# Kernel optimization log

Hardware: AMD Instinct MI355X
Metric: run time of the kernel (lower is better)

Reference implementation:

```python
import jax, jax.numpy as jnp
import numpy as np


def setup_inputs() -> dict:
    key = jax.random.key(0)
    k = jax.random.split(key, 6)
    B, S, L, V = 512, 256, 128, 32000
    words = jax.random.randint(k[0], (B, S), 0, V)
    encoder_emits = jax.random.normal(k[1], (B, S, L), dtype=jnp.float32)
    mask = jnp.ones((B, S), dtype=bool)  # token 0 always valid; all-valid lengths here
    feature_table = jax.random.normal(k[2], (V, L), dtype=jnp.float32)
    start = jax.random.normal(k[3], (L,), dtype=jnp.float32)
    transitions = jax.random.normal(k[4], (L, L), dtype=jnp.float32)
    end = jax.random.normal(k[5], (L,), dtype=jnp.float32)
    return {"words": words, "encoder_emits": encoder_emits, "mask": mask,
            "feature_table": feature_table, "start": start,
            "transitions": transitions, "end": end}


def reference(words, encoder_emits, mask, feature_table, start, transitions, end):
    # decoder emits: feature_scorer(words) modeled as per-word label-score lookup
    dec = feature_table[words]                       # [B, S, L]
    # init at t = 0
    log_alpha = start[None, :] + encoder_emits[:, 0]  # [B, L]
    log_beta = log_alpha + dec[:, 0]                  # [B, L]

    def step(carry, xs):
        la, lb = carry
        e_i, d_i, m_i = xs                            # [B,L], [B,L], [B]
        crf = e_i[:, None, :] + transitions[None]     # [B, L, L] (prev, cur)
        a_new = jax.nn.logsumexp(la[:, :, None] + crf, axis=1)
        b_new = jax.nn.logsumexp(lb[:, :, None] + crf + d_i[:, None, :], axis=1)
        m = m_i[:, None]
        return (jnp.where(m, a_new, la), jnp.where(m, b_new, lb)), None

    xs = (jnp.swapaxes(encoder_emits[:, 1:], 0, 1),   # [S-1, B, L]
          jnp.swapaxes(dec[:, 1:], 0, 1),
          mask[:, 1:].T)                              # [S-1, B]
    (log_alpha, log_beta), _ = jax.lax.scan(step, (log_alpha, log_beta), xs)

    la = jax.nn.logsumexp(log_alpha + end[None, :], axis=-1)  # [B]
    lb = jax.nn.logsumexp(log_beta + end[None, :], axis=-1)   # [B]
    return (la - lb).sum()
```

## Files before the change

kernel.cpp:

```cpp
#include <hip/hip_runtime.h>


constexpr int SS  = 256;
constexpr int LL  = 128;
constexpr int BST = 136;

typedef _Float16 half2_t __attribute__((ext_vector_type(2)));
typedef _Float16 half4_t __attribute__((ext_vector_type(4)));
typedef _Float16 half8_t __attribute__((ext_vector_type(8)));
typedef float    f32x4   __attribute__((ext_vector_type(4)));
typedef unsigned uint2_t __attribute__((ext_vector_type(2)));

#define MFMA16(a, b, c) __builtin_amdgcn_mfma_f32_16x16x32_f16((a), (b), (c), 0, 0, 0)
#define PKRTZ(a, b) __builtin_bit_cast(half2_t, __builtin_amdgcn_cvt_pkrtz((a), (b)))

#define BAR() do {                                                \
    asm volatile("s_waitcnt lgkmcnt(0)" ::: "memory");            \
    __builtin_amdgcn_s_barrier();                                 \
    asm volatile("" ::: "memory");                                \
} while (0)

__device__ __forceinline__ float quad_allmax(float x) {
#if __has_builtin(__builtin_amdgcn_permlane16_swap) && __has_builtin(__builtin_amdgcn_permlane32_swap)
    unsigned u = __builtin_bit_cast(unsigned, x);
    uint2_t a = __builtin_amdgcn_permlane16_swap(u, u, false, false);
    float m = fmaxf(__builtin_bit_cast(float, a.x), __builtin_bit_cast(float, a.y));
    unsigned v = __builtin_bit_cast(unsigned, m);
    uint2_t b = __builtin_amdgcn_permlane32_swap(v, v, false, false);
    return fmaxf(__builtin_bit_cast(float, b.x), __builtin_bit_cast(float, b.y));
#else
    x = fmaxf(x, __shfl_xor(x, 16, 64));
    return fmaxf(x, __shfl_xor(x, 32, 64));
#endif
}

__global__ __launch_bounds__(256) void prepass(
    const int* __restrict__ words, const float* __restrict__ emits,
    const float* __restrict__ ftab,
    half4_t* __restrict__ xe, half4_t* __restrict__ xb,
    float* __restrict__ out)
{
    if (blockIdx.x == 0 && threadIdx.x == 0) *out = 0.f;
    const int t = threadIdx.x;
    const int R = blockIdx.x * 8 + (t >> 5);
    const int c = t & 31;
    const int w = words[R];
    const f32x4 e = *(const f32x4*)&emits[(size_t)R * LL + 4 * c];
    const f32x4 d = *(const f32x4*)&ftab[(size_t)w * LL + 4 * c];
    half4_t a, bb;
    #pragma unroll
    for (int r = 0; r < 4; ++r) {
        a[r]  = (_Float16)__expf(e[r]);
        bb[r] = (_Float16)__expf(e[r] + d[r]);
    }
    xe[(size_t)R * 32 + c] = a;
    xb[(size_t)R * 32 + c] = bb;
}

#define STEP(i, XS) do {                                                      \
    const int rp_ = ((i) + 1) & 1, wp_ = (i) & 1;                             \
    O2 -= __log2f(invp);             \
    half8_t bf_[4];                                                           \
    _Pragma("unroll")                                                         \
    for (int c = 0; c < 4; ++c)                                               \
        bf_[c] = *(const half8_t*)&P[rp_][m15 * BST + c * 32 + quad * 8];     \
    f32x4 a_ = MFMA16(areg[0], bf_[0], zero4);                                \
    f32x4 b_ = MFMA16(areg[2], bf_[2], zero4);                                \
    a_ = MFMA16(areg[1], bf_[1], a_);                                         \
    b_ = MFMA16(areg[3], bf_[3], b_);                                         \
    const f32x4 y_ = a_ + b_;                                                 \
    const float p0_ = y_[0] * (float)XS[0] * invp;                            \
    const float p1_ = y_[1] * (float)XS[1] * invp;                            \
    const float p2_ = y_[2] * (float)XS[2] * invp;                            \
    const float p3_ = y_[3] * (float)XS[3] * invp;                            \
    {                                                                         \
        half2_t h0_ = PKRTZ(p0_, p1_), h1_ = PKRTZ(p2_, p3_);                 \
        half4_t pa_; pa_[0]=h0_[0]; pa_[1]=h0_[1]; pa_[2]=h1_[0]; pa_[3]=h1_[1];\
        *(half4_t*)&P[wp_][m15 * BST + wave * 16 + col0] = pa_;               \
    }                                                                         \
    const int ipf_ = ((i) + 3 < SS) ? (i) + 3 : SS - 1;                       \
    XS = *(const half4_t*)&X[xrow + (size_t)ipf_ * LL + wave * 16 + col0];    \
    float mm_ = fmaxf(fmaxf(p0_, p1_), fmaxf(p2_, p3_));                      \
    mm_ = quad_allmax(mm_);                                                   \
    if (quad == 0) PM[wp_][m15][wave] = mm_;                                  \
    BAR();                                                                    \
    const f32x4 pmA_ = *(const f32x4*)&PM[wp_][m15][0];                       \
    const f32x4 pmB_ = *(const f32x4*)&PM[wp_][m15][4];                       \
    invp = __builtin_amdgcn_rcpf(                                             \
        fmaxf(fmaxf(fmaxf(pmA_[0], pmA_[1]), fmaxf(pmA_[2], pmA_[3])),        \
              fmaxf(fmaxf(pmB_[0], pmB_[1]), fmaxf(pmB_[2], pmB_[3]))));      \
} while (0)

__global__ __launch_bounds__(512, 1) void crf_scan(
    const float* __restrict__ start,
    const float* __restrict__ trans,
    const float* __restrict__ endv,
    const _Float16* __restrict__ xe,
    const _Float16* __restrict__ xb,
    float* __restrict__ out)
{
    const int blk   = blockIdx.x;
    const int chain = blk & 1;
    const int grp   = blk >> 1;
    const int tid   = threadIdx.x;
    const int wave  = tid >> 6;
    const int lane  = tid & 63;
    const int m15   = lane & 15;
    const int quad  = lane >> 4;
    const int col0  = quad * 4;
    const int batch = grp * 16 + m15;
    const _Float16* __restrict__ X = chain ? xb : xe;

    __shared__ __align__(16) _Float16 P[2][16 * BST];
    __shared__ __align__(16) float    PM[2][16][8];

    half8_t areg[4];
    #pragma unroll
    for (int c = 0; c < 4; ++c)
        #pragma unroll
        for (int jj = 0; jj < 8; ++jj)
            areg[c][jj] = (_Float16)__expf(
                trans[(c * 32 + quad * 8 + jj) * LL + wave * 16 + m15]);

    const size_t xrow = (size_t)batch * SS * LL;
    const f32x4 zero4 = (f32x4){0.f, 0.f, 0.f, 0.f};

    float invp, O2 = 0.f;

    {
        const int s0 = wave * 16 + col0;
        const f32x4  sv = *(const f32x4*)&start[s0];
        const half4_t x0 = *(const half4_t*)&X[xrow + s0];
        float y0 = __expf(sv[0]) * (float)x0[0];
        float y1 = __expf(sv[1]) * (float)x0[1];
        float y2 = __expf(sv[2]) * (float)x0[2];
        float y3 = __expf(sv[3]) * (float)x0[3];
        half2_t h0 = PKRTZ(y0, y1), h1 = PKRTZ(y2, y3);
        half4_t pa; pa[0]=h0[0]; pa[1]=h0[1]; pa[2]=h1[0]; pa[3]=h1[1];
        *(half4_t*)&P[0][m15 * BST + s0] = pa;
        float mm = fmaxf(fmaxf(y0, y1), fmaxf(y2, y3));
        mm = quad_allmax(mm);
        if (quad == 0) PM[0][m15][wave] = mm;
    }
    BAR();
    {
        const f32x4 pmA = *(const f32x4*)&PM[0][m15][0];
        const f32x4 pmB = *(const f32x4*)&PM[0][m15][4];
        invp = __builtin_amdgcn_rcpf(
            fmaxf(fmaxf(fmaxf(pmA[0], pmA[1]), fmaxf(pmA[2], pmA[3])),
                  fmaxf(fmaxf(pmB[0], pmB[1]), fmaxf(pmB[2], pmB[3]))));
    }

    half4_t xA, xB, xC;
    xA = *(const half4_t*)&X[xrow + (size_t)1 * LL + wave * 16 + col0];
    xB = *(const half4_t*)&X[xrow + (size_t)2 * LL + wave * 16 + col0];
    xC = *(const half4_t*)&X[xrow + (size_t)3 * LL + wave * 16 + col0];

    for (int i = 1; i + 2 < SS; i += 3) {
        STEP(i,     xA);
        STEP(i + 1, xB);
        STEP(i + 2, xC);
    }

    if (wave == 0) {
        float s = 0.f;
        #pragma unroll
        for (int t = 0; t < 8; ++t) {
            const half4_t p  = *(const half4_t*)&P[1][m15 * BST + t * 16 + col0];
            const f32x4   ev = *(const f32x4*)&endv[t * 16 + col0];
            #pragma unroll
            for (int r = 0; r < 4; ++r)
                s += (float)p[r] * __expf(ev[r]);
        }
        s += __shfl_xor(s, 16, 64);
        s += __shfl_xor(s, 32, 64);
        float lf = O2 * 0.6931471805599453f + __logf(s);
        if (chain) lf = -lf;
        if (quad == 0) {
            lf += __shfl_xor(lf, 1, 64);
            lf += __shfl_xor(lf, 2, 64);
            lf += __shfl_xor(lf, 4, 64);
            lf += __shfl_xor(lf, 8, 64);
            if (m15 == 0) atomicAdd(out, lf);
        }
    }
}

extern "C" void kernel_launch(void* const* d_in, const int* in_sizes, int n_in,
                              void* d_out, int out_size, void* d_ws, size_t ws_size,
                              hipStream_t stream) {
    const int*   words = (const int*)d_in[0];
    const float* emits = (const float*)d_in[1];
    const float* ftab  = (const float*)d_in[3];
    const float* start = (const float*)d_in[4];
    const float* trans = (const float*)d_in[5];
    const float* endv  = (const float*)d_in[6];
    float* out = (float*)d_out;

    half4_t* xe = (half4_t*)d_ws;
    half4_t* xb = xe + (size_t)512 * SS * 32;

    prepass<<<512 * SS / 8, 256, 0, stream>>>(words, emits, ftab, xe, xb, out);
    crf_scan<<<64, 512, 0, stream>>>(start, trans, endv,
                                     (const _Float16*)xe, (const _Float16*)xb, out);
}
```

Baseline: 222.1 us.

## Split batch across more blocks with four sequences per MFMA tile

Each scan block now handles 4 batch rows instead of 16, and the launch grows from 64 to 256 blocks so more compute units work on the sequential CRF recurrence. The MFMA still runs on 16 rows, with rows replicated modulo 4, so three quarters of the matrix work is redundant but the per-step latency stays about the same. The aim is to use more CUs at once; in exchange the per-batch transition matrix loads and the redundant MFMA work add overhead, and the LDS row stride changes to 144.

```diff
diff --git a/kernel.cpp b/kernel.cpp
--- a/kernel.cpp
+++ b/kernel.cpp
@@ -3,7 +3,8 @@
 
 constexpr int SS  = 256;
 constexpr int LL  = 128;
-constexpr int BST = 136;
+constexpr int BB  = 4;
+constexpr int BST = 144;
 
 typedef _Float16 half2_t __attribute__((ext_vector_type(2)));
 typedef _Float16 half4_t __attribute__((ext_vector_type(4)));
@@ -63,7 +64,7 @@
     half8_t bf_[4];                                                           \
     _Pragma("unroll")                                                         \
     for (int c = 0; c < 4; ++c)                                               \
-        bf_[c] = *(const half8_t*)&P[rp_][m15 * BST + c * 32 + quad * 8];     \
+        bf_[c] = *(const half8_t*)&P[rp_][bsl * BST + c * 32 + quad * 8];     \
     f32x4 a_ = MFMA16(areg[0], bf_[0], zero4);                                \
     f32x4 b_ = MFMA16(areg[2], bf_[2], zero4);                                \
     a_ = MFMA16(areg[1], bf_[1], a_);                                         \
@@ -73,7 +74,7 @@
     const float p1_ = y_[1] * (float)XS[1] * invp;                            \
     const float p2_ = y_[2] * (float)XS[2] * invp;                            \
     const float p3_ = y_[3] * (float)XS[3] * invp;                            \
-    {                                                                         \
+    if (m15 < BB) {                                                           \
         half2_t h0_ = PKRTZ(p0_, p1_), h1_ = PKRTZ(p2_, p3_);                 \
         half4_t pa_; pa_[0]=h0_[0]; pa_[1]=h0_[1]; pa_[2]=h1_[0]; pa_[3]=h1_[1];\
         *(half4_t*)&P[wp_][m15 * BST + wave * 16 + col0] = pa_;               \
@@ -82,10 +83,10 @@
     XS = *(const half4_t*)&X[xrow + (size_t)ipf_ * LL + wave * 16 + col0];    \
     float mm_ = fmaxf(fmaxf(p0_, p1_), fmaxf(p2_, p3_));                      \
     mm_ = quad_allmax(mm_);                                                   \
-    if (quad == 0) PM[wp_][m15][wave] = mm_;                                  \
+    if (quad == 0 && m15 < BB) PM[wp_][m15][wave] = mm_;                      \
     BAR();                                                                    \
-    const f32x4 pmA_ = *(const f32x4*)&PM[wp_][m15][0];                       \
-    const f32x4 pmB_ = *(const f32x4*)&PM[wp_][m15][4];                       \
+    const f32x4 pmA_ = *(const f32x4*)&PM[wp_][bsl][0];                       \
+    const f32x4 pmB_ = *(const f32x4*)&PM[wp_][bsl][4];                       \
     invp = __builtin_amdgcn_rcpf(                                             \
         fmaxf(fmaxf(fmaxf(pmA_[0], pmA_[1]), fmaxf(pmA_[2], pmA_[3])),        \
               fmaxf(fmaxf(pmB_[0], pmB_[1]), fmaxf(pmB_[2], pmB_[3]))));      \
@@ -106,13 +107,14 @@
     const int wave  = tid >> 6;
     const int lane  = tid & 63;
     const int m15   = lane & 15;
+    const int bsl   = m15 & (BB - 1);
     const int quad  = lane >> 4;
     const int col0  = quad * 4;
-    const int batch = grp * 16 + m15;
+    const int batch = grp * BB + bsl;
     const _Float16* __restrict__ X = chain ? xb : xe;
 
-    __shared__ __align__(16) _Float16 P[2][16 * BST];
-    __shared__ __align__(16) float    PM[2][16][8];
+    __shared__ __align__(16) _Float16 P[2][BB * BST];
+    __shared__ __align__(16) float    PM[2][BB][8];
 
     half8_t areg[4];
     #pragma unroll
@@ -135,17 +137,19 @@
         float y1 = __expf(sv[1]) * (float)x0[1];
         float y2 = __expf(sv[2]) * (float)x0[2];
         float y3 = __expf(sv[3]) * (float)x0[3];
-        half2_t h0 = PKRTZ(y0, y1), h1 = PKRTZ(y2, y3);
-        half4_t pa; pa[0]=h0[0]; pa[1]=h0[1]; pa[2]=h1[0]; pa[3]=h1[1];
-        *(half4_t*)&P[0][m15 * BST + s0] = pa;
+        if (m15 < BB) {
+            half2_t h0 = PKRTZ(y0, y1), h1 = PKRTZ(y2, y3);
+            half4_t pa; pa[0]=h0[0]; pa[1]=h0[1]; pa[2]=h1[0]; pa[3]=h1[1];
+            *(half4_t*)&P[0][m15 * BST + s0] = pa;
+        }
         float mm = fmaxf(fmaxf(y0, y1), fmaxf(y2, y3));
         mm = quad_allmax(mm);
-        if (quad == 0) PM[0][m15][wave] = mm;
+        if (quad == 0 && m15 < BB) PM[0][m15][wave] = mm;
     }
     BAR();
     {
-        const f32x4 pmA = *(const f32x4*)&PM[0][m15][0];
-        const f32x4 pmB = *(const f32x4*)&PM[0][m15][4];
+        const f32x4 pmA = *(const f32x4*)&PM[0][bsl][0];
+        const f32x4 pmB = *(const f32x4*)&PM[0][bsl][4];
         invp = __builtin_amdgcn_rcpf(
             fmaxf(fmaxf(fmaxf(pmA[0], pmA[1]), fmaxf(pmA[2], pmA[3])),
                   fmaxf(fmaxf(pmB[0], pmB[1]), fmaxf(pmB[2], pmB[3]))));
@@ -166,7 +170,7 @@
         float s = 0.f;
         #pragma unroll
         for (int t = 0; t < 8; ++t) {
-            const half4_t p  = *(const half4_t*)&P[1][m15 * BST + t * 16 + col0];
+            const half4_t p  = *(const half4_t*)&P[1][bsl * BST + t * 16 + col0];
             const f32x4   ev = *(const f32x4*)&endv[t * 16 + col0];
             #pragma unroll
             for (int r = 0; r < 4; ++r)
@@ -179,8 +183,6 @@
         if (quad == 0) {
             lf += __shfl_xor(lf, 1, 64);
             lf += __shfl_xor(lf, 2, 64);
-            lf += __shfl_xor(lf, 4, 64);
-            lf += __shfl_xor(lf, 8, 64);
             if (m15 == 0) atomicAdd(out, lf);
         }
     }
@@ -201,6 +203,6 @@
     half4_t* xb = xe + (size_t)512 * SS * 32;
 
     prepass<<<512 * SS / 8, 256, 0, stream>>>(words, emits, ftab, xe, xb, out);
-    crf_scan<<<64, 512, 0, stream>>>(start, trans, endv,
-                                     (const _Float16*)xe, (const _Float16*)xb, out);
-}
+    crf_scan<<<256, 512, 0, stream>>>(start, trans, endv,
+                                      (const _Float16*)xe, (const _Float16*)xb, out);
+}
```

New measurement: 221.0 us. No clear change (-0.5%).

## Run each CRF chain group in a single wave with register-resident state

Applied to the files above, without the earlier changes.

Replaces the 8-wave block, which exchanged the state vector through LDS with a barrier every step, with a single 64-lane wave. That wave holds all 128x128 transition tiles in registers (32 half8 fragments per lane) and issues 32 MFMAs per step. The permuted source-row mapping lets the MFMA output layout be repacked directly as the next step's B operand, so no LDS or barriers are needed. In exchange, each wave does 8x the MFMA work serially, uses only 64 waves GPU-wide, and carries heavy register pressure.

```diff
diff --git a/kernel.cpp b/kernel.cpp
--- a/kernel.cpp
+++ b/kernel.cpp
@@ -1,9 +1,8 @@
 #include <hip/hip_runtime.h>
 
 
-constexpr int SS  = 256;
-constexpr int LL  = 128;
-constexpr int BST = 136;
+constexpr int SS = 256;
+constexpr int LL = 128;
 
 typedef _Float16 half2_t __attribute__((ext_vector_type(2)));
 typedef _Float16 half4_t __attribute__((ext_vector_type(4)));
@@ -13,12 +12,6 @@
 
 #define MFMA16(a, b, c) __builtin_amdgcn_mfma_f32_16x16x32_f16((a), (b), (c), 0, 0, 0)
 #define PKRTZ(a, b) __builtin_bit_cast(half2_t, __builtin_amdgcn_cvt_pkrtz((a), (b)))
-
-#define BAR() do {                                                \
-    asm volatile("s_waitcnt lgkmcnt(0)" ::: "memory");            \
-    __builtin_amdgcn_s_barrier();                                 \
-    asm volatile("" ::: "memory");                                \
-} while (0)
 
 __device__ __forceinline__ float quad_allmax(float x) {
 #if __has_builtin(__builtin_amdgcn_permlane16_swap) && __has_builtin(__builtin_amdgcn_permlane32_swap)
@@ -58,40 +51,42 @@
 }
 
 #define STEP(i, XS) do {                                                      \
-    const int rp_ = ((i) + 1) & 1, wp_ = (i) & 1;                             \
     O2 -= __log2f(invp);             \
-    half8_t bf_[4];                                                           \
-    _Pragma("unroll")                                                         \
-    for (int c = 0; c < 4; ++c)                                               \
-        bf_[c] = *(const half8_t*)&P[rp_][m15 * BST + c * 32 + quad * 8];     \
-    f32x4 a_ = MFMA16(areg[0], bf_[0], zero4);                                \
-    f32x4 b_ = MFMA16(areg[2], bf_[2], zero4);                                \
-    a_ = MFMA16(areg[1], bf_[1], a_);                                         \
-    b_ = MFMA16(areg[3], bf_[3], b_);                                         \
-    const f32x4 y_ = a_ + b_;                                                 \
-    const float p0_ = y_[0] * (float)XS[0] * invp;                            \
-    const float p1_ = y_[1] * (float)XS[1] * invp;                            \
-    const float p2_ = y_[2] * (float)XS[2] * invp;                            \
-    const float p3_ = y_[3] * (float)XS[3] * invp;                            \
-    {                                                                         \
-        half2_t h0_ = PKRTZ(p0_, p1_), h1_ = PKRTZ(p2_, p3_);                 \
-        half4_t pa_; pa_[0]=h0_[0]; pa_[1]=h0_[1]; pa_[2]=h1_[0]; pa_[3]=h1_[1];\
-        *(half4_t*)&P[wp_][m15 * BST + wave * 16 + col0] = pa_;               \
+    f32x4 acc_[8];                                                            \
+    _Pragma("unroll")                                                         \
+    for (int t = 0; t < 8; ++t)                                               \
+        acc_[t] = MFMA16(areg[t][0], bf[0], zero4);                           \
+    _Pragma("unroll")                                                         \
+    for (int c = 1; c < 4; ++c) {                                             \
+        _Pragma("unroll")                                                     \
+        for (int t = 0; t < 8; ++t)                                           \
+            acc_[t] = MFMA16(areg[t][c], bf[c], acc_[t]);                     \
     }                                                                         \
-    const int ipf_ = ((i) + 3 < SS) ? (i) + 3 : SS - 1;                       \
-    XS = *(const half4_t*)&X[xrow + (size_t)ipf_ * LL + wave * 16 + col0];    \
-    float mm_ = fmaxf(fmaxf(p0_, p1_), fmaxf(p2_, p3_));                      \
+    float mm_ = -3.0e38f;                                                     \
+    half8_t nbf_[4];                                                          \
+    _Pragma("unroll")                                                         \
+    for (int t = 0; t < 8; ++t) {                                             \
+        const int hi_ = t >> 1, e0_ = (t & 1) * 4;                            \
+        const float p0_ = acc_[t][0] * (float)XS[hi_][e0_ + 0] * invp;        \
+        const float p1_ = acc_[t][1] * (float)XS[hi_][e0_ + 1] * invp;        \
+        const float p2_ = acc_[t][2] * (float)XS[hi_][e0_ + 2] * invp;        \
+        const float p3_ = acc_[t][3] * (float)XS[hi_][e0_ + 3] * invp;        \
+        mm_ = fmaxf(mm_, fmaxf(fmaxf(p0_, p1_), fmaxf(p2_, p3_)));            \
+        const half2_t h0_ = PKRTZ(p0_, p1_), h1_ = PKRTZ(p2_, p3_);           \
+        nbf_[hi_][e0_ + 0] = h0_[0]; nbf_[hi_][e0_ + 1] = h0_[1];             \
+        nbf_[hi_][e0_ + 2] = h1_[0]; nbf_[hi_][e0_ + 3] = h1_[1];             \
+    }                                                                         \
+    _Pragma("unroll")                                                         \
+    for (int c = 0; c < 4; ++c) bf[c] = nbf_[c];                              \
+    const int ipf_ = ((i) + 2 < SS) ? (i) + 2 : SS - 1;                       \
+    _Pragma("unroll")                                                         \
+    for (int hi = 0; hi < 4; ++hi)                                            \
+        XS[hi] = *(const half8_t*)&X[xrow + (size_t)ipf_ * LL + hi * 32 + quad * 8];\
     mm_ = quad_allmax(mm_);                                                   \
-    if (quad == 0) PM[wp_][m15][wave] = mm_;                                  \
-    BAR();                                                                    \
-    const f32x4 pmA_ = *(const f32x4*)&PM[wp_][m15][0];                       \
-    const f32x4 pmB_ = *(const f32x4*)&PM[wp_][m15][4];                       \
-    invp = __builtin_amdgcn_rcpf(                                             \
-        fmaxf(fmaxf(fmaxf(pmA_[0], pmA_[1]), fmaxf(pmA_[2], pmA_[3])),        \
-              fmaxf(fmaxf(pmB_[0], pmB_[1]), fmaxf(pmB_[2], pmB_[3]))));      \
+    invp = __builtin_amdgcn_rcpf(mm_);                                        \
 } while (0)
 
-__global__ __launch_bounds__(512, 1) void crf_scan(
+__global__ __launch_bounds__(64, 1) void crf_scan(
     const float* __restrict__ start,
     const float* __restrict__ trans,
     const float* __restrict__ endv,
@@ -102,87 +97,88 @@
     const int blk   = blockIdx.x;
     const int chain = blk & 1;
     const int grp   = blk >> 1;
-    const int tid   = threadIdx.x;
-    const int wave  = tid >> 6;
-    const int lane  = tid & 63;
+    const int lane  = threadIdx.x;
     const int m15   = lane & 15;
     const int quad  = lane >> 4;
-    const int col0  = quad * 4;
     const int batch = grp * 16 + m15;
     const _Float16* __restrict__ X = chain ? xb : xe;
 
-    __shared__ __align__(16) _Float16 P[2][16 * BST];
-    __shared__ __align__(16) float    PM[2][16][8];
-
-    half8_t areg[4];
-    #pragma unroll
-    for (int c = 0; c < 4; ++c)
-        #pragma unroll
-        for (int jj = 0; jj < 8; ++jj)
-            areg[c][jj] = (_Float16)__expf(
-                trans[(c * 32 + quad * 8 + jj) * LL + wave * 16 + m15]);
+    half8_t areg[8][4];
+    #pragma unroll
+    for (int t = 0; t < 8; ++t) {
+        const int srow = (t >> 1) * 32 + (m15 >> 2) * 8 + (t & 1) * 4 + (m15 & 3);
+        #pragma unroll
+        for (int c = 0; c < 4; ++c)
+            #pragma unroll
+            for (int jj = 0; jj < 8; ++jj)
+                areg[t][c][jj] = (_Float16)__expf(
+                    trans[(c * 32 + quad * 8 + jj) * LL + srow]);
+    }
 
     const size_t xrow = (size_t)batch * SS * LL;
     const f32x4 zero4 = (f32x4){0.f, 0.f, 0.f, 0.f};
 
+    half8_t bf[4];
     float invp, O2 = 0.f;
 
     {
-        const int s0 = wave * 16 + col0;
-        const f32x4  sv = *(const f32x4*)&start[s0];
-        const half4_t x0 = *(const half4_t*)&X[xrow + s0];
-        float y0 = __expf(sv[0]) * (float)x0[0];
-        float y1 = __expf(sv[1]) * (float)x0[1];
-        float y2 = __expf(sv[2]) * (float)x0[2];
-        float y3 = __expf(sv[3]) * (float)x0[3];
-        half2_t h0 = PKRTZ(y0, y1), h1 = PKRTZ(y2, y3);
-        half4_t pa; pa[0]=h0[0]; pa[1]=h0[1]; pa[2]=h1[0]; pa[3]=h1[1];
-        *(half4_t*)&P[0][m15 * BST + s0] = pa;
-        float mm = fmaxf(fmaxf(y0, y1), fmaxf(y2, y3));
+        float mm = -3.0e38f;
+        #pragma unroll
+        for (int c = 0; c < 4; ++c) {
+            const int j0 = c * 32 + quad * 8;
+            const f32x4  s0 = *(const f32x4*)&start[j0];
+            const f32x4  s1 = *(const f32x4*)&start[j0 + 4];
+            const half8_t x0 = *(const half8_t*)&X[xrow + j0];
+            float y[8];
+            #pragma unroll
+            for (int r = 0; r < 4; ++r) y[r]     = __expf(s0[r]) * (float)x0[r];
+            #pragma unroll
+            for (int r = 0; r < 4; ++r) y[4 + r] = __expf(s1[r]) * (float)x0[4 + r];
+            #pragma unroll
+            for (int r = 0; r < 8; ++r) mm = fmaxf(mm, y[r]);
+            const half2_t h0 = PKRTZ(y[0], y[1]), h1 = PKRTZ(y[2], y[3]);
+            const half2_t h2 = PKRTZ(y[4], y[5]), h3 = PKRTZ(y[6], y[7]);
+            bf[c][0] = h0[0]; bf[c][1] = h0[1]; bf[c][2] = h1[0]; bf[c][3] = h1[1];
+            bf[c][4] = h2[0]; bf[c][5] = h2[1]; bf[c][6] = h3[0]; bf[c][7] = h3[1];
+        }
         mm = quad_allmax(mm);
-        if (quad == 0) PM[0][m15][wave] = mm;
-    }
-    BAR();
-    {
-        const f32x4 pmA = *(const f32x4*)&PM[0][m15][0];
-        const f32x4 pmB = *(const f32x4*)&PM[0][m15][4];
-        invp = __builtin_amdgcn_rcpf(
-            fmaxf(fmaxf(fmaxf(pmA[0], pmA[1]), fmaxf(pmA[2], pmA[3])),
-                  fmaxf(fmaxf(pmB[0], pmB[1]), fmaxf(pmB[2], pmB[3]))));
-    }
-
-    half4_t xA, xB, xC;
-    xA = *(const half4_t*)&X[xrow + (size_t)1 * LL + wave * 16 + col0];
-    xB = *(const half4_t*)&X[xrow + (size_t)2 * LL + wave * 16 + col0];
-    xC = *(const half4_t*)&X[xrow + (size_t)3 * LL + wave * 16 + col0];
-
-    for (int i = 1; i + 2 < SS; i += 3) {
+        invp = __builtin_amdgcn_rcpf(mm);
+    }
+
+    half8_t xA[4], xB[4];
+    #pragma unroll
+    for (int hi = 0; hi < 4; ++hi) {
+        xA[hi] = *(const half8_t*)&X[xrow + (size_t)1 * LL + hi * 32 + quad * 8];
+        xB[hi] = *(const half8_t*)&X[xrow + (size_t)2 * LL + hi * 32 + quad * 8];
+    }
+
+    for (int i = 1; i + 1 < SS; i += 2) {
         STEP(i,     xA);
         STEP(i + 1, xB);
-        STEP(i + 2, xC);
-    }
-
-    if (wave == 0) {
-        float s = 0.f;
-        #pragma unroll
-        for (int t = 0; t < 8; ++t) {
-            const half4_t p  = *(const half4_t*)&P[1][m15 * BST + t * 16 + col0];
-            const f32x4   ev = *(const f32x4*)&endv[t * 16 + col0];
-            #pragma unroll
-            for (int r = 0; r < 4; ++r)
-                s += (float)p[r] * __expf(ev[r]);
-        }
-        s += __shfl_xor(s, 16, 64);
-        s += __shfl_xor(s, 32, 64);
-        float lf = O2 * 0.6931471805599453f + __logf(s);
-        if (chain) lf = -lf;
-        if (quad == 0) {
-            lf += __shfl_xor(lf, 1, 64);
-            lf += __shfl_xor(lf, 2, 64);
-            lf += __shfl_xor(lf, 4, 64);
-            lf += __shfl_xor(lf, 8, 64);
-            if (m15 == 0) atomicAdd(out, lf);
-        }
+    }
+    STEP(SS - 1, xA);
+
+    float s = 0.f;
+    #pragma unroll
+    for (int c = 0; c < 4; ++c) {
+        const int j0 = c * 32 + quad * 8;
+        const f32x4 e0 = *(const f32x4*)&endv[j0];
+        const f32x4 e1 = *(const f32x4*)&endv[j0 + 4];
+        #pragma unroll
+        for (int r = 0; r < 4; ++r) s += (float)bf[c][r]     * __expf(e0[r]);
+        #pragma unroll
+        for (int r = 0; r < 4; ++r) s += (float)bf[c][4 + r] * __expf(e1[r]);
+    }
+    s += __shfl_xor(s, 16, 64);
+    s += __shfl_xor(s, 32, 64);
+    float lf = O2 * 0.6931471805599453f + __logf(s);
+    if (chain) lf = -lf;
+    if (quad == 0) {
+        lf += __shfl_xor(lf, 1, 64);
+        lf += __shfl_xor(lf, 2, 64);
+        lf += __shfl_xor(lf, 4, 64);
+        lf += __shfl_xor(lf, 8, 64);
+        if (m15 == 0) atomicAdd(out, lf);
     }
 }
 
@@ -201,6 +197,6 @@
     half4_t* xb = xe + (size_t)512 * SS * 32;
 
     prepass<<<512 * SS / 8, 256, 0, stream>>>(words, emits, ftab, xe, xb, out);
-    crf_scan<<<64, 512, 0, stream>>>(start, trans, endv,
-                                     (const _Float16*)xe, (const _Float16*)xb, out);
-}
+    crf_scan<<<64, 64, 0, stream>>>(start, trans, endv,
+                                    (const _Float16*)xe, (const _Float16*)xb, out);
+}
```

Measured after the change: 330.7 us. +48.9%, slower.
